# Kernel tuning notes

Hardware: AMD Instinct MI355X
Metric: run time of the kernel (lower is better)

The kernel has to match this reference:

```python
import jax, jax.numpy as jnp
import numpy as np

N_WORDS, N_SENTS = 200_000, 20_000
IN_DIM, OUT_DIM, FEAT = 128, 64, 50
N_EDGES = 2_000_000
NEG_SLOPE = 0.01  # torch F.leaky_relu default


def setup_inputs() -> dict:
    key = jax.random.key(0)
    k = jax.random.split(key, 7)
    h = jax.random.normal(k[0], (N_WORDS + N_SENTS, IN_DIM), dtype=jnp.float32)
    tfidf = jax.random.normal(k[1], (N_EDGES, FEAT), dtype=jnp.float32)
    W_fc = jax.random.normal(k[2], (OUT_DIM, IN_DIM), dtype=jnp.float32) / np.sqrt(IN_DIM)
    W_feat = jax.random.normal(k[3], (OUT_DIM, FEAT), dtype=jnp.float32) / np.sqrt(FEAT)
    W_attn = jax.random.normal(k[4], (1, 3 * OUT_DIM), dtype=jnp.float32) / np.sqrt(3 * OUT_DIM)
    src = jax.random.randint(k[5], (N_EDGES,), 0, N_WORDS, dtype=jnp.int32)
    dst = jax.random.randint(k[6], (N_EDGES,), 0, N_SENTS, dtype=jnp.int32)
    return {"h": h, "tfidf": tfidf, "W_fc": W_fc, "W_feat": W_feat,
            "W_attn": W_attn, "src": src, "dst": dst, "n_sents": N_SENTS}


def reference(h, tfidf, W_fc, W_feat, W_attn, src, dst, n_sents):
    n_words = h.shape[0] - n_sents
    out_dim = W_fc.shape[0]
    z = h @ W_fc.T                                  # [N, D]
    z_src = z[src]                                  # [E, D] gather word z
    z_dst = z[n_words + dst]                        # [E, D] gather sentence z
    dfeat = tfidf @ W_feat.T                        # [E, D] feat_fc
    wa = W_attn[0]                                  # [3D]; concat+linear == split dot
    e = z_src @ wa[:out_dim] + z_dst @ wa[out_dim:2 * out_dim] + dfeat @ wa[2 * out_dim:]
    e = jnp.where(e >= 0, e, NEG_SLOPE * e)         # leaky_relu, [E]
    # segment softmax over each sentence's incoming edges
    m = jax.ops.segment_max(e, dst, num_segments=n_sents)
    m = jnp.where(jnp.isfinite(m), m, 0.0)          # guard empty segments
    ex = jnp.exp(e - m[dst])
    denom = jax.ops.segment_sum(ex, dst, num_segments=n_sents)
    alpha = ex / denom[dst]                         # [E]
    # weighted scatter-sum of source features
    sh = jax.ops.segment_sum(alpha[:, None] * z_src, dst, num_segments=n_sents)
    return sh                                       # [n_sents, D]
```

## Files before the change

### kernel.cpp

```cpp
#include <hip/hip_runtime.h>
#include <hip/hip_bf16.h>
#include <hip/hip_fp16.h>
#include <cstdint>

#define IN_DIM 128
#define OUT_DIM 64
#define FEATD 50
#define NEG_SLOPE 0.01f

typedef unsigned int uint32;
typedef _Float16 half4 __attribute__((ext_vector_type(4)));
typedef float f32x4 __attribute__((ext_vector_type(4)));

__global__ __launch_bounds__(256) void k_v3zero(const float* __restrict__ W_feat,
                                                const float* __restrict__ W_attn,
                                                float* __restrict__ v3,
                                                uint32* __restrict__ cnt,
                                                int n_sents) {
  int i = blockIdx.x * 256 + threadIdx.x;
  if (i < n_sents) cnt[i] = 0u;
  if (blockIdx.x == 0 && threadIdx.x < FEATD) {
    int j = threadIdx.x;
    float s = 0.f;
    #pragma unroll
    for (int o = 0; o < OUT_DIM; ++o)
      s = fmaf(W_attn[2 * OUT_DIM + o], W_feat[o * FEATD + j], s);
    v3[j] = s;
  }
}

__global__ __launch_bounds__(256) void k_node_mfma(const float* __restrict__ h,
    const float* __restrict__ W_fc, const float* __restrict__ W_attn,
    __half* __restrict__ z, float* __restrict__ s1, float* __restrict__ s2,
    int n_words, int n_nodes) {
  __shared__ float zl[4][16][68];
  int w = threadIdx.x >> 6, lane = threadIdx.x & 63;
  int nb = blockIdx.x * 64 + w * 16;
  int lrow = lane & 15;
  int lk4 = (lane >> 4) * 4;

  int an = nb + lrow;
  if (an >= n_nodes) an = n_nodes - 1;
  const float* hrow = h + (size_t)an * IN_DIM;

  f32x4 acc[4];
  #pragma unroll
  for (int nt = 0; nt < 4; ++nt) acc[nt] = (f32x4){0.f, 0.f, 0.f, 0.f};

  #pragma unroll
  for (int ks = 0; ks < 8; ++ks) {
    float4 hv = *(const float4*)(hrow + ks * 16 + lk4);
    half4 a;
    a[0] = (_Float16)hv.x; a[1] = (_Float16)hv.y;
    a[2] = (_Float16)hv.z; a[3] = (_Float16)hv.w;
    #pragma unroll
    for (int nt = 0; nt < 4; ++nt) {
      const float* wrow = W_fc + (size_t)(nt * 16 + lrow) * IN_DIM + ks * 16 + lk4;
      float4 wv = *(const float4*)wrow;
      half4 b;
      b[0] = (_Float16)wv.x; b[1] = (_Float16)wv.y;
      b[2] = (_Float16)wv.z; b[3] = (_Float16)wv.w;
      acc[nt] = __builtin_amdgcn_mfma_f32_16x16x16f16(a, b, acc[nt], 0, 0, 0);
    }
  }

  int drow = (lane >> 4) * 4;
  #pragma unroll
  for (int nt = 0; nt < 4; ++nt)
    #pragma unroll
    for (int r = 0; r < 4; ++r)
      zl[w][drow + r][nt * 16 + lrow] = acc[nt][r];

  int node = lane >> 2;
  int chunk = lane & 3;
  float v[16];
  #pragma unroll
  for (int q = 0; q < 4; ++q) {
    float4 t = *(const float4*)&zl[w][node][chunk * 16 + q * 4];
    v[4 * q + 0] = t.x; v[4 * q + 1] = t.y;
    v[4 * q + 2] = t.z; v[4 * q + 3] = t.w;
  }

  int gn = nb + node;
  bool valid = gn < n_nodes;
  bool isword = gn < n_words;
  const float* wa = W_attn + (isword ? 0 : OUT_DIM) + chunk * 16;
  float p = 0.f;
  #pragma unroll
  for (int t = 0; t < 16; ++t) p = fmaf(v[t], wa[t], p);
  p += __shfl_xor(p, 1);
  p += __shfl_xor(p, 2);

  if (valid && chunk == 0) {
    if (isword) s1[gn] = p; else s2[gn - n_words] = p;
  }
  if (valid && isword) {
    uint32 d[8];
    #pragma unroll
    for (int k = 0; k < 8; ++k) {
      __half2 t = __floats2half2_rn(v[2 * k], v[2 * k + 1]);
      d[k] = *(uint32*)&t;
    }
    uint4* dstp = (uint4*)(z + (size_t)gn * OUT_DIM + chunk * 16);
    dstp[0] = make_uint4(d[0], d[1], d[2], d[3]);
    dstp[1] = make_uint4(d[4], d[5], d[6], d[7]);
  }
}

__global__ __launch_bounds__(256) void k_hist(const int* __restrict__ dst,
                                              uint32* __restrict__ cnt,
                                              uint32* __restrict__ rank, int E) {
  int e = blockIdx.x * 256 + threadIdx.x;
  if (e < E) rank[e] = atomicAdd(&cnt[dst[e]], 1u);
}

__global__ __launch_bounds__(1024) void k_scan(const uint32* __restrict__ cnt,
    uint32* __restrict__ off, int n) {
  __shared__ uint32 part[1024];
  int t = threadIdx.x;
  int CH = (n + 1023) >> 10;
  int base = t * CH;
  uint32 s = 0;
  for (int k = 0; k < CH; ++k) { int i = base + k; if (i < n) s += cnt[i]; }
  part[t] = s;
  __syncthreads();
  uint32 x = s;
  for (int d = 1; d < 1024; d <<= 1) {
    uint32 v = (t >= d) ? part[t - d] : 0u;
    __syncthreads();
    x += v;
    part[t] = x;
    __syncthreads();
  }
  uint32 run = (t > 0) ? part[t - 1] : 0u;
  for (int k = 0; k < CH; ++k) {
    int i = base + k;
    if (i < n) { off[i] = run; run += cnt[i]; }
  }
  if (t == 1023) off[n] = part[1023];
}

__global__ __launch_bounds__(256) void k_edge(const float* __restrict__ tfidf,
    const int* __restrict__ src, const int* __restrict__ dst,
    const float* __restrict__ s1, const float* __restrict__ s2,
    const float* __restrict__ v3, const uint32* __restrict__ off,
    const uint32* __restrict__ rank, float2* __restrict__ pair, int E) {
  int e = blockIdx.x * 256 + threadIdx.x;
  if (e >= E) return;
  const float* row = tfidf + (size_t)e * FEATD;
  float f = 0.f;
  #pragma unroll
  for (int k = 0; k < FEATD / 2; ++k) {
    float2 v = *(const float2*)(row + 2 * k);
    f = fmaf(v.x, v3[2 * k], f);
    f = fmaf(v.y, v3[2 * k + 1], f);
  }
  int sidx = src[e], d = dst[e];
  float ev = s1[sidx] + s2[d] + f;
  ev = ev >= 0.f ? ev : NEG_SLOPE * ev;
  float exv = __expf(ev);
  float2 pr;
  pr.x = exv;
  pr.y = __int_as_float(sidx);
  pair[off[d] + rank[e]] = pr;
}

__global__ __launch_bounds__(256) void k_agg(const __half* __restrict__ z,
    const float2* __restrict__ pair, const uint32* __restrict__ off,
    float* __restrict__ out, int n_sents) {
  int w = threadIdx.x >> 6, lane = threadIdx.x & 63;
  int s = blockIdx.x * 4 + w;
  if (s >= n_sents) return;
  uint32 j0 = off[s], j1 = off[s + 1];
  int sub = lane >> 4;
  int d4 = (lane & 15) * 4;

  float a0 = 0.f, a1 = 0.f, a2 = 0.f, a3 = 0.f, sa = 0.f;
  uint32 b = j0;
  for (; b + 32 <= j1; b += 32) {
    float2 p[8];
    #pragma unroll
    for (int k = 0; k < 8; ++k) p[k] = pair[b + 4 * k + sub];
    uint2 u[8];
    #pragma unroll
    for (int k = 0; k < 8; ++k) {
      uint32 sv = (uint32)__float_as_int(p[k].y);
      u[k] = *(const uint2*)(z + (size_t)sv * OUT_DIM + d4);
    }
    #pragma unroll
    for (int k = 0; k < 8; ++k) {
      float al = p[k].x;
      __half2 h01 = *(__half2*)&u[k].x;
      __half2 h23 = *(__half2*)&u[k].y;
      a0 = fmaf(al, __low2float(h01), a0);
      a1 = fmaf(al, __high2float(h01), a1);
      a2 = fmaf(al, __low2float(h23), a2);
      a3 = fmaf(al, __high2float(h23), a3);
      sa += al;
    }
  }
  for (; b + 4 <= j1; b += 4) {
    float2 p = pair[b + sub];
    uint32 sv = (uint32)__float_as_int(p.y);
    uint2 u = *(const uint2*)(z + (size_t)sv * OUT_DIM + d4);
    float al = p.x;
    __half2 h01 = *(__half2*)&u.x;
    __half2 h23 = *(__half2*)&u.y;
    a0 = fmaf(al, __low2float(h01), a0);
    a1 = fmaf(al, __high2float(h01), a1);
    a2 = fmaf(al, __low2float(h23), a2);
    a3 = fmaf(al, __high2float(h23), a3);
    sa += al;
  }
  if (sub < (int)(j1 - b)) {
    float2 p = pair[b + sub];
    uint32 sv = (uint32)__float_as_int(p.y);
    uint2 u = *(const uint2*)(z + (size_t)sv * OUT_DIM + d4);
    float al = p.x;
    __half2 h01 = *(__half2*)&u.x;
    __half2 h23 = *(__half2*)&u.y;
    a0 = fmaf(al, __low2float(h01), a0);
    a1 = fmaf(al, __high2float(h01), a1);
    a2 = fmaf(al, __low2float(h23), a2);
    a3 = fmaf(al, __high2float(h23), a3);
    sa += al;
  }

  a0 += __shfl_xor(a0, 16); a0 += __shfl_xor(a0, 32);
  a1 += __shfl_xor(a1, 16); a1 += __shfl_xor(a1, 32);
  a2 += __shfl_xor(a2, 16); a2 += __shfl_xor(a2, 32);
  a3 += __shfl_xor(a3, 16); a3 += __shfl_xor(a3, 32);
  sa += __shfl_xor(sa, 16); sa += __shfl_xor(sa, 32);

  if (sub == 0) {
    float inv = (sa > 0.f) ? (1.f / sa) : 0.f;
    float4 o;
    o.x = a0 * inv; o.y = a1 * inv; o.z = a2 * inv; o.w = a3 * inv;
    *(float4*)(out + (size_t)s * OUT_DIM + d4) = o;
  }
}

extern "C" void kernel_launch(void* const* d_in, const int* in_sizes, int n_in,
                              void* d_out, int out_size, void* d_ws, size_t ws_size,
                              hipStream_t stream) {
  const float* h      = (const float*)d_in[0];
  const float* tfidf  = (const float*)d_in[1];
  const float* W_fc   = (const float*)d_in[2];
  const float* W_feat = (const float*)d_in[3];
  const float* W_attn = (const float*)d_in[4];
  const int*   src    = (const int*)d_in[5];
  const int*   dst    = (const int*)d_in[6];

  int n_nodes = in_sizes[0] / IN_DIM;
  int E       = in_sizes[5];
  int n_sents = out_size / OUT_DIM;
  int n_words = n_nodes - n_sents;
  float* out = (float*)d_out;

  char* ws = (char*)d_ws;
  size_t ofs = 0;
  auto alloc = [&](size_t bytes) -> char* {
    char* p = ws + ofs;
    ofs += (bytes + 255) / 256 * 256;
    return p;
  };
  __half* z      = (__half*)alloc((size_t)n_words * OUT_DIM * 2);
  float*  s1     = (float*)alloc((size_t)n_words * 4);
  float*  s2     = (float*)alloc((size_t)n_sents * 4);
  float2* pair   = (float2*)alloc((size_t)E * 8);
  uint32* rank   = (uint32*)alloc((size_t)E * 4);
  uint32* cnt    = (uint32*)alloc((size_t)n_sents * 4);
  uint32* offs   = (uint32*)alloc((size_t)(n_sents + 1) * 4);
  float*  v3     = (float*)alloc(FEATD * 4);
  (void)ws_size; (void)n_in;

  k_v3zero<<<(n_sents + 255) / 256, 256, 0, stream>>>(W_feat, W_attn, v3, cnt,
                                                      n_sents);
  k_node_mfma<<<(n_nodes + 63) / 64, 256, 0, stream>>>(h, W_fc, W_attn, z, s1,
                                                       s2, n_words, n_nodes);
  k_hist<<<(E + 255) / 256, 256, 0, stream>>>(dst, cnt, rank, E);
  k_scan<<<1, 1024, 0, stream>>>(cnt, offs, n_sents);
  k_edge<<<(E + 255) / 256, 256, 0, stream>>>(tfidf, src, dst, s1, s2, v3,
                                              offs, rank, pair, E);
  k_agg<<<(n_sents + 3) / 4, 256, 0, stream>>>(z, pair, offs, out, n_sents);
}
```

Before: 382.4 us.

## Bucket edges by source-word chunk per sentence and aggregate per chunk

```diff
diff --git a/kernel.cpp b/kernel.cpp
--- a/kernel.cpp
+++ b/kernel.cpp
@@ -7,18 +7,19 @@
 #define OUT_DIM 64
 #define FEATD 50
 #define NEG_SLOPE 0.01f
+#define NCH 8
 
 typedef unsigned int uint32;
 typedef _Float16 half4 __attribute__((ext_vector_type(4)));
 typedef float f32x4 __attribute__((ext_vector_type(4)));
 
-__global__ __launch_bounds__(256) void k_v3zero(const float* __restrict__ W_feat,
-                                                const float* __restrict__ W_attn,
-                                                float* __restrict__ v3,
-                                                uint32* __restrict__ cnt,
-                                                int n_sents) {
+__global__ __launch_bounds__(256) void k_init(const float* __restrict__ W_feat,
+                                              const float* __restrict__ W_attn,
+                                              float* __restrict__ v3,
+                                              uint32* __restrict__ cnt,
+                                              int ncnt) {
   int i = blockIdx.x * 256 + threadIdx.x;
-  if (i < n_sents) cnt[i] = 0u;
+  if (i < ncnt) cnt[i] = 0u;
   if (blockIdx.x == 0 && threadIdx.x < FEATD) {
     int j = threadIdx.x;
     float s = 0.f;
@@ -108,43 +109,75 @@
 }
 
 __global__ __launch_bounds__(256) void k_hist(const int* __restrict__ dst,
+                                              const int* __restrict__ src,
                                               uint32* __restrict__ cnt,
-                                              uint32* __restrict__ rank, int E) {
-  int e = blockIdx.x * 256 + threadIdx.x;
-  if (e < E) rank[e] = atomicAdd(&cnt[dst[e]], 1u);
-}
-
-__global__ __launch_bounds__(1024) void k_scan(const uint32* __restrict__ cnt,
-    uint32* __restrict__ off, int n) {
+                                              uint32* __restrict__ rank,
+                                              int E, uint32 cw) {
+  int i = blockIdx.x * 256 + threadIdx.x;
+  int e0 = i * 2;
+  if (e0 + 1 < E) {
+    int2 d2 = *(const int2*)(dst + e0);
+    int2 s2 = *(const int2*)(src + e0);
+    uint32 c0 = (uint32)s2.x / cw, c1 = (uint32)s2.y / cw;
+    uint32 r0 = atomicAdd(&cnt[(uint32)d2.x * NCH + c0], 1u);
+    uint32 r1 = atomicAdd(&cnt[(uint32)d2.y * NCH + c1], 1u);
+    *(uint2*)(rank + e0) = make_uint2(r0, r1);
+  } else if (e0 < E) {
+    uint32 c0 = (uint32)src[e0] / cw;
+    rank[e0] = atomicAdd(&cnt[(uint32)dst[e0] * NCH + c0], 1u);
+  }
+}
+
+__global__ __launch_bounds__(1024) void k_scanA(const uint32* __restrict__ cnt,
+    uint32* __restrict__ off, uint32* __restrict__ btot, int n) {
   __shared__ uint32 part[1024];
   int t = threadIdx.x;
-  int CH = (n + 1023) >> 10;
-  int base = t * CH;
-  uint32 s = 0;
-  for (int k = 0; k < CH; ++k) { int i = base + k; if (i < n) s += cnt[i]; }
-  part[t] = s;
+  int i = blockIdx.x * 1024 + t;
+  uint32 v = (i < n) ? cnt[i] : 0u;
+  part[t] = v;
   __syncthreads();
-  uint32 x = s;
+  uint32 x = v;
   for (int d = 1; d < 1024; d <<= 1) {
-    uint32 v = (t >= d) ? part[t - d] : 0u;
+    uint32 y = (t >= d) ? part[t - d] : 0u;
     __syncthreads();
-    x += v;
+    x += y;
     part[t] = x;
     __syncthreads();
   }
-  uint32 run = (t > 0) ? part[t - 1] : 0u;
-  for (int k = 0; k < CH; ++k) {
-    int i = base + k;
-    if (i < n) { off[i] = run; run += cnt[i]; }
-  }
-  if (t == 1023) off[n] = part[1023];
+  if (i < n) off[i] = x - v;
+  if (t == 1023) btot[blockIdx.x] = x;
+}
+__global__ __launch_bounds__(1024) void k_scanB(const uint32* __restrict__ btot,
+                                                uint32* __restrict__ boff, int nb) {
+  __shared__ uint32 part[1024];
+  int t = threadIdx.x;
+  uint32 v = (t < nb) ? btot[t] : 0u;
+  part[t] = v;
+  __syncthreads();
+  uint32 x = v;
+  for (int d = 1; d < 1024; d <<= 1) {
+    uint32 y = (t >= d) ? part[t - d] : 0u;
+    __syncthreads();
+    x += y;
+    part[t] = x;
+    __syncthreads();
+  }
+  if (t < nb) boff[t] = x - v;
+  if (t == 1023) boff[nb] = x;
+}
+__global__ __launch_bounds__(1024) void k_scanC(uint32* __restrict__ off,
+    const uint32* __restrict__ boff, int n, int nb) {
+  int i = blockIdx.x * 1024 + threadIdx.x;
+  if (i < n) off[i] += boff[i >> 10];
+  if (i == 0) off[n] = boff[nb];
 }
 
 __global__ __launch_bounds__(256) void k_edge(const float* __restrict__ tfidf,
     const int* __restrict__ src, const int* __restrict__ dst,
     const float* __restrict__ s1, const float* __restrict__ s2,
     const float* __restrict__ v3, const uint32* __restrict__ off,
-    const uint32* __restrict__ rank, float2* __restrict__ pair, int E) {
+    const uint32* __restrict__ rank, float2* __restrict__ pair, int E,
+    uint32 cw) {
   int e = blockIdx.x * 256 + threadIdx.x;
   if (e >= E) return;
   const float* row = tfidf + (size_t)e * FEATD;
@@ -162,68 +195,62 @@
   float2 pr;
   pr.x = exv;
   pr.y = __int_as_float(sidx);
-  pair[off[d] + rank[e]] = pr;
-}
-
-__global__ __launch_bounds__(256) void k_agg(const __half* __restrict__ z,
+  uint32 c = (uint32)sidx / cw;
+  pair[off[(uint32)d * NCH + c] + rank[e]] = pr;
+}
+
+__global__ __launch_bounds__(256) void k_aggp(const __half* __restrict__ z,
     const float2* __restrict__ pair, const uint32* __restrict__ off,
-    float* __restrict__ out, int n_sents) {
+    float* __restrict__ pout, float* __restrict__ psum, int n_sents) {
   int w = threadIdx.x >> 6, lane = threadIdx.x & 63;
-  int s = blockIdx.x * 4 + w;
+  int c = blockIdx.x & (NCH - 1);
+  int g = blockIdx.x / NCH;
+  int s = g * 4 + w;
   if (s >= n_sents) return;
-  uint32 j0 = off[s], j1 = off[s + 1];
+  int seg = s * NCH + c;
+  uint32 j0 = off[seg], j1 = off[seg + 1];
   int sub = lane >> 4;
   int d4 = (lane & 15) * 4;
 
   float a0 = 0.f, a1 = 0.f, a2 = 0.f, a3 = 0.f, sa = 0.f;
   uint32 b = j0;
-  for (; b + 32 <= j1; b += 32) {
-    float2 p[8];
-    #pragma unroll
-    for (int k = 0; k < 8; ++k) p[k] = pair[b + 4 * k + sub];
-    uint2 u[8];
-    #pragma unroll
-    for (int k = 0; k < 8; ++k) {
-      uint32 sv = (uint32)__float_as_int(p[k].y);
-      u[k] = *(const uint2*)(z + (size_t)sv * OUT_DIM + d4);
-    }
-    #pragma unroll
-    for (int k = 0; k < 8; ++k) {
-      float al = p[k].x;
-      __half2 h01 = *(__half2*)&u[k].x;
-      __half2 h23 = *(__half2*)&u[k].y;
-      a0 = fmaf(al, __low2float(h01), a0);
-      a1 = fmaf(al, __high2float(h01), a1);
-      a2 = fmaf(al, __low2float(h23), a2);
-      a3 = fmaf(al, __high2float(h23), a3);
-      sa += al;
-    }
+  for (; b + 8 <= j1; b += 8) {
+    float2 p0 = pair[b + sub];
+    float2 p1 = pair[b + 4 + sub];
+    uint2 u0 = *(const uint2*)(z + (size_t)(uint32)__float_as_int(p0.y) * OUT_DIM + d4);
+    uint2 u1 = *(const uint2*)(z + (size_t)(uint32)__float_as_int(p1.y) * OUT_DIM + d4);
+    __half2 h01 = *(__half2*)&u0.x, h23 = *(__half2*)&u0.y;
+    a0 = fmaf(p0.x, __low2float(h01), a0);
+    a1 = fmaf(p0.x, __high2float(h01), a1);
+    a2 = fmaf(p0.x, __low2float(h23), a2);
+    a3 = fmaf(p0.x, __high2float(h23), a3);
+    sa += p0.x;
+    __half2 g01 = *(__half2*)&u1.x, g23 = *(__half2*)&u1.y;
+    a0 = fmaf(p1.x, __low2float(g01), a0);
+    a1 = fmaf(p1.x, __high2float(g01), a1);
+    a2 = fmaf(p1.x, __low2float(g23), a2);
+    a3 = fmaf(p1.x, __high2float(g23), a3);
+    sa += p1.x;
   }
   for (; b + 4 <= j1; b += 4) {
     float2 p = pair[b + sub];
-    uint32 sv = (uint32)__float_as_int(p.y);
-    uint2 u = *(const uint2*)(z + (size_t)sv * OUT_DIM + d4);
-    float al = p.x;
-    __half2 h01 = *(__half2*)&u.x;
-    __half2 h23 = *(__half2*)&u.y;
-    a0 = fmaf(al, __low2float(h01), a0);
-    a1 = fmaf(al, __high2float(h01), a1);
-    a2 = fmaf(al, __low2float(h23), a2);
-    a3 = fmaf(al, __high2float(h23), a3);
-    sa += al;
+    uint2 u = *(const uint2*)(z + (size_t)(uint32)__float_as_int(p.y) * OUT_DIM + d4);
+    __half2 h01 = *(__half2*)&u.x, h23 = *(__half2*)&u.y;
+    a0 = fmaf(p.x, __low2float(h01), a0);
+    a1 = fmaf(p.x, __high2float(h01), a1);
+    a2 = fmaf(p.x, __low2float(h23), a2);
+    a3 = fmaf(p.x, __high2float(h23), a3);
+    sa += p.x;
   }
   if (sub < (int)(j1 - b)) {
     float2 p = pair[b + sub];
-    uint32 sv = (uint32)__float_as_int(p.y);
-    uint2 u = *(const uint2*)(z + (size_t)sv * OUT_DIM + d4);
-    float al = p.x;
-    __half2 h01 = *(__half2*)&u.x;
-    __half2 h23 = *(__half2*)&u.y;
-    a0 = fmaf(al, __low2float(h01), a0);
-    a1 = fmaf(al, __high2float(h01), a1);
-    a2 = fmaf(al, __low2float(h23), a2);
-    a3 = fmaf(al, __high2float(h23), a3);
-    sa += al;
+    uint2 u = *(const uint2*)(z + (size_t)(uint32)__float_as_int(p.y) * OUT_DIM + d4);
+    __half2 h01 = *(__half2*)&u.x, h23 = *(__half2*)&u.y;
+    a0 = fmaf(p.x, __low2float(h01), a0);
+    a1 = fmaf(p.x, __high2float(h01), a1);
+    a2 = fmaf(p.x, __low2float(h23), a2);
+    a3 = fmaf(p.x, __high2float(h23), a3);
+    sa += p.x;
   }
 
   a0 += __shfl_xor(a0, 16); a0 += __shfl_xor(a0, 32);
@@ -233,11 +260,25 @@
   sa += __shfl_xor(sa, 16); sa += __shfl_xor(sa, 32);
 
   if (sub == 0) {
-    float inv = (sa > 0.f) ? (1.f / sa) : 0.f;
     float4 o;
-    o.x = a0 * inv; o.y = a1 * inv; o.z = a2 * inv; o.w = a3 * inv;
-    *(float4*)(out + (size_t)s * OUT_DIM + d4) = o;
-  }
+    o.x = a0; o.y = a1; o.z = a2; o.w = a3;
+    *(float4*)(pout + (size_t)seg * OUT_DIM + d4) = o;
+    if (lane == 0) psum[seg] = sa;
+  }
+}
+
+__global__ __launch_bounds__(256) void k_combine(const float* __restrict__ pout,
+    const float* __restrict__ psum, float* __restrict__ out, int n_sents) {
+  int w = threadIdx.x >> 6, lane = threadIdx.x & 63;
+  int s = blockIdx.x * 4 + w;
+  if (s >= n_sents) return;
+  float acc = 0.f, sa = 0.f;
+  #pragma unroll
+  for (int c = 0; c < NCH; ++c) {
+    acc += pout[((size_t)s * NCH + c) * OUT_DIM + lane];
+    sa += psum[s * NCH + c];
+  }
+  out[(size_t)s * OUT_DIM + lane] = (sa > 0.f) ? (acc / sa) : 0.f;
 }
 
 extern "C" void kernel_launch(void* const* d_in, const int* in_sizes, int n_in,
@@ -256,6 +297,10 @@
   int n_sents = out_size / OUT_DIM;
   int n_words = n_nodes - n_sents;
   float* out = (float*)d_out;
+
+  uint32 cw = (uint32)((n_words + NCH - 1) / NCH);
+  int ncnt = n_sents * NCH;
+  int nb = (ncnt + 1023) / 1024;
 
   char* ws = (char*)d_ws;
   size_t ofs = 0;
@@ -269,18 +314,25 @@
   float*  s2     = (float*)alloc((size_t)n_sents * 4);
   float2* pair   = (float2*)alloc((size_t)E * 8);
   uint32* rank   = (uint32*)alloc((size_t)E * 4);
-  uint32* cnt    = (uint32*)alloc((size_t)n_sents * 4);
-  uint32* offs   = (uint32*)alloc((size_t)(n_sents + 1) * 4);
+  uint32* cnt    = (uint32*)alloc((size_t)ncnt * 4);
+  uint32* offs   = (uint32*)alloc((size_t)(ncnt + 1) * 4);
+  uint32* btot   = (uint32*)alloc(1028 * 4);
+  uint32* boff   = (uint32*)alloc(1028 * 4);
+  float*  pout   = (float*)alloc((size_t)ncnt * OUT_DIM * 4);
+  float*  psum   = (float*)alloc((size_t)ncnt * 4);
   float*  v3     = (float*)alloc(FEATD * 4);
   (void)ws_size; (void)n_in;
 
-  k_v3zero<<<(n_sents + 255) / 256, 256, 0, stream>>>(W_feat, W_attn, v3, cnt,
-                                                      n_sents);
+  k_init<<<(ncnt + 255) / 256, 256, 0, stream>>>(W_feat, W_attn, v3, cnt, ncnt);
   k_node_mfma<<<(n_nodes + 63) / 64, 256, 0, stream>>>(h, W_fc, W_attn, z, s1,
                                                        s2, n_words, n_nodes);
-  k_hist<<<(E + 255) / 256, 256, 0, stream>>>(dst, cnt, rank, E);
-  k_scan<<<1, 1024, 0, stream>>>(cnt, offs, n_sents);
+  k_hist<<<(E / 2 + 255) / 256, 256, 0, stream>>>(dst, src, cnt, rank, E, cw);
+  k_scanA<<<nb, 1024, 0, stream>>>(cnt, offs, btot, ncnt);
+  k_scanB<<<1, 1024, 0, stream>>>(btot, boff, nb);
+  k_scanC<<<(ncnt + 1024) / 1024, 1024, 0, stream>>>(offs, boff, ncnt, nb);
   k_edge<<<(E + 255) / 256, 256, 0, stream>>>(tfidf, src, dst, s1, s2, v3,
-                                              offs, rank, pair, E);
-  k_agg<<<(n_sents + 3) / 4, 256, 0, stream>>>(z, pair, offs, out, n_sents);
-}
+                                              offs, rank, pair, E, cw);
+  k_aggp<<<((n_sents + 3) / 4) * NCH, 256, 0, stream>>>(z, pair, offs, pout,
+                                                        psum, n_sents);
+  k_combine<<<(n_sents + 3) / 4, 256, 0, stream>>>(pout, psum, out, n_sents);
+}
```

New measurement: 409.7 us. +7.1%, slower.
